# Kernel tuning notes

Hardware: AMD Instinct MI355X
Metric: run time of the kernel (lower is better)

The kernel has to match this reference:

```python
import jax, jax.numpy as jnp
import numpy as np

DIM = 128
WS = 7
NH = 8
HEAD_DIM = DIM // NH
SCALE = HEAD_DIM ** -0.5


def setup_inputs() -> dict:
    key = jax.random.key(0)
    k1, k2, k3, k4 = jax.random.split(key, 4)
    x = jax.random.normal(k1, (32, 56, 56, DIM), dtype=jnp.float32)
    qkv_w = jax.random.normal(k2, (3 * DIM, DIM), dtype=jnp.float32) * (DIM ** -0.5)
    proj_w = jax.random.normal(k3, (DIM, DIM), dtype=jnp.float32) * (DIM ** -0.5)
    proj_b = jax.random.normal(k4, (DIM,), dtype=jnp.float32) * 0.01
    return {"x": x, "qkv_w": qkv_w, "proj_w": proj_w, "proj_b": proj_b}


def reference(x, qkv_w, proj_w, proj_b):
    B, H, W, C = x.shape
    pad_b = (WS - H % WS) % WS
    pad_r = (WS - W % WS) % WS
    x = jnp.pad(x, ((0, 0), (0, pad_b), (0, pad_r), (0, 0)))
    Hp, Wp = H + pad_b, W + pad_r
    nH, nW = Hp // WS, Wp // WS
    # window partition: [B*nH*nW, WS*WS, C]
    xw = x.reshape(B, nH, WS, nW, WS, C).transpose(0, 1, 3, 2, 4, 5)
    xw = xw.reshape(B * nH * nW, WS * WS, C)
    # qkv projection (torch Linear: x @ W^T), split into heads
    qkv = (xw @ qkv_w.T).reshape(-1, WS * WS, 3, NH, HEAD_DIM)
    qkv = qkv.transpose(2, 0, 3, 1, 4)  # [3, nWin, H, T, d]
    q, k, v = qkv[0], qkv[1], qkv[2]
    attn = jax.nn.softmax(jnp.einsum('nhqd,nhkd->nhqk', q, k) * SCALE, axis=-1)
    out = jnp.einsum('nhqk,nhkd->nhqd', attn, v)
    out = out.transpose(0, 2, 1, 3).reshape(-1, WS * WS, C)
    out = out @ proj_w.T + proj_b
    # window reverse
    out = out.reshape(B, nH, nW, WS, WS, C).transpose(0, 1, 3, 2, 4, 5)
    out = out.reshape(B, Hp, Wp, C)
    return out[:, :H, :W, :]
```

## Files before the change

### kernel.cpp

```cpp
#include <hip/hip_runtime.h>

typedef unsigned short ushort_t;
typedef __attribute__((ext_vector_type(8))) short short8v;
typedef __attribute__((ext_vector_type(4))) short short4v;
typedef __attribute__((ext_vector_type(4))) float f32x4;
typedef __attribute__((ext_vector_type(2))) __bf16 bf16x2;

#define QOFF   0
#define KOFF   8704
#define AOOFF  0
#define VOFF   17408
#define SMEMSZ 26624

__device__ __forceinline__ ushort_t f2bf(float f) {
  return __builtin_bit_cast(unsigned short, (__bf16)f);
}
__device__ __forceinline__ unsigned pack2(float lo, float hi) {
  bf16x2 v; v[0] = (__bf16)lo; v[1] = (__bf16)hi;
  return __builtin_bit_cast(unsigned, v);
}

__device__ __forceinline__ f32x4 mfma16(short8v a, short8v b, f32x4 c) {
  return __builtin_amdgcn_mfma_f32_16x16x32_bf16(a, b, c, 0, 0, 0);
}

template<bool WS>
__device__ __forceinline__ short8v load_w8(const ushort_t* wsp, const float* wf, int n, int k0) {
  if constexpr (WS) {
    return *reinterpret_cast<const short8v*>(wsp + (size_t)n * 128 + k0);
  } else {
    const float* p = wf + (size_t)n * 128 + k0;
    float4 f0 = *reinterpret_cast<const float4*>(p);
    float4 f1 = *reinterpret_cast<const float4*>(p + 4);
    short8v t;
    t[0] = (short)f2bf(f0.x); t[1] = (short)f2bf(f0.y);
    t[2] = (short)f2bf(f0.z); t[3] = (short)f2bf(f0.w);
    t[4] = (short)f2bf(f1.x); t[5] = (short)f2bf(f1.y);
    t[6] = (short)f2bf(f1.z); t[7] = (short)f2bf(f1.w);
    return t;
  }
}

__global__ void cvt_w(const float* __restrict__ qw, const float* __restrict__ pw,
                      ushort_t* __restrict__ ws) {
  const int i = blockIdx.x * 256 + threadIdx.x;
  if (i < 49152) ws[i] = f2bf(qw[i]);
  if (i < 16384) ws[49152 + i] = f2bf(pw[i]);
}

template<bool WS>
__global__ __launch_bounds__(256, 2)
void winattn(const float* __restrict__ xg,
             const float* __restrict__ qw,
             const float* __restrict__ pw,
             const float* __restrict__ pb,
             const ushort_t* __restrict__ wsw,
             float* __restrict__ out) {
  __shared__ ushort_t smem[SMEMSZ];

  const int tid  = threadIdx.x;
  const int wid  = tid >> 6;
  const int lane = tid & 63;
  const int l15  = lane & 15;
  const int quad = lane >> 4;

  const int wb = blockIdx.x;
  const int b  = wb >> 6;
  const int wh = (wb >> 3) & 7;
  const int ww = wb & 7;
  const int rowbase = (b * 56 + wh * 7) * 56 + ww * 7;

  const float bias0 = pb[wid * 32 + l15];
  const float bias1 = pb[wid * 32 + 16 + l15];

  {
    const int tr = tid >> 5;
    const int c4 = tid & 31;
    #pragma unroll
    for (int it = 0; it < 8; ++it) {
      const int t = it * 8 + tr;
      uint2 pk = make_uint2(0u, 0u);
      if (t < 49) {
        const int i = t / 7, j = t - (t / 7) * 7;
        const float4 v = *reinterpret_cast<const float4*>(
            xg + (size_t)(rowbase + i * 56 + j) * 128 + c4 * 4);
        pk.x = pack2(v.x, v.y);
        pk.y = pack2(v.z, v.w);
      }
      *reinterpret_cast<uint2*>(&smem[t * 136 + c4 * 4]) = pk;
    }
  }
  __syncthreads();

  short8v a[4][4];
  #pragma unroll
  for (int qi = 0; qi < 4; ++qi)
    #pragma unroll
    for (int ks = 0; ks < 4; ++ks)
      a[qi][ks] = *reinterpret_cast<const short8v*>(
          &smem[(qi * 16 + l15) * 136 + ks * 32 + quad * 8]);
  __syncthreads();

  #pragma unroll
  for (int pass = 0; pass < 2; ++pass) {
    f32x4 acc[4][3];
    #pragma unroll
    for (int qi = 0; qi < 4; ++qi)
      #pragma unroll
      for (int ni = 0; ni < 3; ++ni)
        acc[qi][ni] = (f32x4){0.f, 0.f, 0.f, 0.f};

    #pragma unroll
    for (int nis = 0; nis < 3; ++nis) {
      const int ni = pass * 3 + nis;
      const int n  = wid * 96 + ni * 16 + l15;
      short8v bf[4];
      #pragma unroll
      for (int ks = 0; ks < 4; ++ks)
        bf[ks] = load_w8<WS>(wsw, qw, n, ks * 32 + quad * 8);
      #pragma unroll
      for (int qi = 0; qi < 4; ++qi)
        #pragma unroll
        for (int ks = 0; ks < 4; ++ks)
          acc[qi][nis] = mfma16(a[qi][ks], bf[ks], acc[qi][nis]);
    }

    #pragma unroll
    for (int nis = 0; nis < 3; ++nis) {
      const int ni    = pass * 3 + nis;
      const int obase = wid * 96 + ni * 16;
      if (obase < 256) {
        const int colo = ((obase < 128) ? QOFF : (KOFF - 128)) + obase + l15;
        #pragma unroll
        for (int qi = 0; qi < 4; ++qi)
          #pragma unroll
          for (int r = 0; r < 4; ++r)
            smem[colo + (qi * 16 + quad * 4 + r) * 136] = f2bf(acc[qi][nis][r]);
      } else {
        const int vrow = obase - 256 + l15;
        #pragma unroll
        for (int qi = 0; qi < 4; ++qi) {
          uint2 pk;
          pk.x = pack2(acc[qi][nis][0], acc[qi][nis][1]);
          pk.y = pack2(acc[qi][nis][2], acc[qi][nis][3]);
          *reinterpret_cast<uint2*>(&smem[VOFF + vrow * 72 + qi * 16 + quad * 4]) = pk;
        }
      }
    }
  }
  __syncthreads();

  f32x4 s[2][4][4];
  #pragma unroll
  for (int hh = 0; hh < 2; ++hh) {
    const int h    = wid * 2 + hh;
    const int colb = h * 16 + (quad & 1) * 8;
    const bool act = quad < 2;
    short8v aq[4], bk[4];
    #pragma unroll
    for (int qi = 0; qi < 4; ++qi) {
      short8v v = *reinterpret_cast<const short8v*>(&smem[QOFF + (qi * 16 + l15) * 136 + colb]);
      aq[qi] = act ? v : (short8v)0;
    }
    #pragma unroll
    for (int ki = 0; ki < 4; ++ki) {
      short8v v = *reinterpret_cast<const short8v*>(&smem[KOFF + (ki * 16 + l15) * 136 + colb]);
      bk[ki] = act ? v : (short8v)0;
    }
    #pragma unroll
    for (int qi = 0; qi < 4; ++qi)
      #pragma unroll
      for (int ki = 0; ki < 4; ++ki)
        s[hh][qi][ki] = mfma16(aq[qi], bk[ki], (f32x4){0.f, 0.f, 0.f, 0.f});
  }

  const float cexp = 0.3606737602222409f;
  #pragma unroll
  for (int hh = 0; hh < 2; ++hh) {
    #pragma unroll
    for (int qi = 0; qi < 4; ++qi) {
      #pragma unroll
      for (int r = 0; r < 4; ++r)
        s[hh][qi][3][r] = (l15 >= 1) ? -1e30f : s[hh][qi][3][r];
      #pragma unroll
      for (int r = 0; r < 4; ++r) {
        float sum = 0.f;
        #pragma unroll
        for (int ki = 0; ki < 4; ++ki) {
          const float e = __builtin_amdgcn_exp2f(s[hh][qi][ki][r] * cexp);
          s[hh][qi][ki][r] = e;
          sum += e;
        }
        sum += __shfl_xor(sum, 1);
        sum += __shfl_xor(sum, 2);
        sum += __shfl_xor(sum, 4);
        sum += __shfl_xor(sum, 8);
        const float rs = __builtin_amdgcn_rcpf(sum);
        #pragma unroll
        for (int ki = 0; ki < 4; ++ki) s[hh][qi][ki][r] *= rs;
      }
    }
  }
  __syncthreads();

  const int pbase = wid * 4352;
  f32x4 ov[2][4];
  #pragma unroll
  for (int hh = 0; hh < 2; ++hh) {
    #pragma unroll
    for (int qi = 0; qi < 4; ++qi)
      #pragma unroll
      for (int ki = 0; ki < 4; ++ki)
        #pragma unroll
        for (int r = 0; r < 4; ++r)
          smem[pbase + (qi * 16 + quad * 4 + r) * 68 + ki * 16 + l15] = f2bf(s[hh][qi][ki][r]);

    const int h = wid * 2 + hh;
    short8v bv[2];
    #pragma unroll
    for (int ks = 0; ks < 2; ++ks)
      bv[ks] = *reinterpret_cast<const short8v*>(
          &smem[VOFF + (h * 16 + l15) * 72 + ks * 32 + quad * 8]);
    #pragma unroll
    for (int qi = 0; qi < 4; ++qi) {
      f32x4 acc = (f32x4){0.f, 0.f, 0.f, 0.f};
      #pragma unroll
      for (int ks = 0; ks < 2; ++ks) {
        const ushort_t* pp = &smem[pbase + (qi * 16 + l15) * 68 + ks * 32 + quad * 8];
        const short4v p0 = *reinterpret_cast<const short4v*>(pp);
        const short4v p1 = *reinterpret_cast<const short4v*>(pp + 4);
        const short8v ap = {p0[0], p0[1], p0[2], p0[3], p1[0], p1[1], p1[2], p1[3]};
        acc = mfma16(ap, bv[ks], acc);
      }
      ov[hh][qi] = acc;
    }
  }
  __syncthreads();

  #pragma unroll
  for (int hh = 0; hh < 2; ++hh) {
    const int c = (wid * 2 + hh) * 16 + l15;
    #pragma unroll
    for (int qi = 0; qi < 4; ++qi)
      #pragma unroll
      for (int r = 0; r < 4; ++r)
        smem[AOOFF + (qi * 16 + quad * 4 + r) * 136 + c] = f2bf(ov[hh][qi][r]);
  }
  __syncthreads();

  short8v aa[4][4];
  #pragma unroll
  for (int qi = 0; qi < 4; ++qi)
    #pragma unroll
    for (int ks = 0; ks < 4; ++ks)
      aa[qi][ks] = *reinterpret_cast<const short8v*>(
          &smem[AOOFF + (qi * 16 + l15) * 136 + ks * 32 + quad * 8]);

  f32x4 pacc[4][2];
  #pragma unroll
  for (int qi = 0; qi < 4; ++qi)
    #pragma unroll
    for (int ni = 0; ni < 2; ++ni)
      pacc[qi][ni] = (f32x4){0.f, 0.f, 0.f, 0.f};

  #pragma unroll
  for (int ni = 0; ni < 2; ++ni) {
    const int n = wid * 32 + ni * 16 + l15;
    short8v bf[4];
    #pragma unroll
    for (int ks = 0; ks < 4; ++ks)
      bf[ks] = load_w8<WS>(wsw + 49152, pw, n, ks * 32 + quad * 8);
    #pragma unroll
    for (int qi = 0; qi < 4; ++qi)
      #pragma unroll
      for (int ks = 0; ks < 4; ++ks)
        pacc[qi][ni] = mfma16(aa[qi][ks], bf[ks], pacc[qi][ni]);
  }

  #pragma unroll
  for (int qi = 0; qi < 4; ++qi) {
    #pragma unroll
    for (int r = 0; r < 4; ++r) {
      const int q = qi * 16 + quad * 4 + r;
      if (q < 49) {
        const int i = q / 7, j = q - (q / 7) * 7;
        float* op = out + (size_t)(rowbase + i * 56 + j) * 128 + wid * 32 + l15;
        op[0]  = pacc[qi][0][r] + bias0;
        op[16] = pacc[qi][1][r] + bias1;
      }
    }
  }
}

extern "C" void kernel_launch(void* const* d_in, const int* in_sizes, int n_in,
                              void* d_out, int out_size, void* d_ws, size_t ws_size,
                              hipStream_t stream) {
  const float* x  = (const float*)d_in[0];
  const float* qw = (const float*)d_in[1];
  const float* pw = (const float*)d_in[2];
  const float* pb = (const float*)d_in[3];
  float* out      = (float*)d_out;
  ushort_t* ws    = (ushort_t*)d_ws;

  const bool use_ws = (ws_size >= (size_t)(49152 + 16384) * sizeof(ushort_t));
  if (use_ws) {
    hipLaunchKernelGGL(cvt_w, dim3(192), dim3(256), 0, stream, qw, pw, ws);
    hipLaunchKernelGGL((winattn<true>), dim3(2048), dim3(256), 0, stream,
                       x, qw, pw, pb, ws, out);
  } else {
    hipLaunchKernelGGL((winattn<false>), dim3(2048), dim3(256), 0, stream,
                       x, qw, pw, pb, (const ushort_t*)nullptr, out);
  }
}
```

Baseline: 164.7 us.

## Compute S^T via swapped MFMA operands and route softmax probabilities through lane shuffles

Swaps the QK^T MFMA operands so each lane holds a query's scores along keys, which reduces the softmax row-sum to two cross-lane shuffles. The normalized probabilities are packed to bf16 and redistributed with register shuffles into the A-operand layout for the PV MFMA, so they no longer round-trip through shared memory. This removes a block-wide barrier and the LDS write and read of P, and fuses the QK, softmax and PV stages per query tile. In exchange it adds many ds_bpermute shuffles and select instructions per tile, and the key-padding mask logic is rewritten for the transposed layout.

```diff
diff --git a/kernel.cpp b/kernel.cpp
--- a/kernel.cpp
+++ b/kernel.cpp
@@ -2,7 +2,7 @@
 
 typedef unsigned short ushort_t;
 typedef __attribute__((ext_vector_type(8))) short short8v;
-typedef __attribute__((ext_vector_type(4))) short short4v;
+typedef __attribute__((ext_vector_type(4))) int   i32x4;
 typedef __attribute__((ext_vector_type(4))) float f32x4;
 typedef __attribute__((ext_vector_type(2))) __bf16 bf16x2;
 
@@ -150,89 +150,83 @@
   }
   __syncthreads();
 
-  f32x4 s[2][4][4];
+  const float cexp = 0.3606737602222409f;
+  const int srcA = l15 + ((quad & 1) << 5);
+  const int srcB = srcA + 16;
+  const bool loq = (quad < 2);
+
+  f32x4 ov[2][4];
   #pragma unroll
   for (int hh = 0; hh < 2; ++hh) {
     const int h    = wid * 2 + hh;
     const int colb = h * 16 + (quad & 1) * 8;
     const bool act = quad < 2;
-    short8v aq[4], bk[4];
+    short8v bk[4], aq[4], bv[2];
+    #pragma unroll
+    for (int ki = 0; ki < 4; ++ki) {
+      short8v v = *reinterpret_cast<const short8v*>(&smem[KOFF + (ki * 16 + l15) * 136 + colb]);
+      bk[ki] = act ? v : (short8v)0;
+    }
     #pragma unroll
     for (int qi = 0; qi < 4; ++qi) {
       short8v v = *reinterpret_cast<const short8v*>(&smem[QOFF + (qi * 16 + l15) * 136 + colb]);
       aq[qi] = act ? v : (short8v)0;
     }
     #pragma unroll
-    for (int ki = 0; ki < 4; ++ki) {
-      short8v v = *reinterpret_cast<const short8v*>(&smem[KOFF + (ki * 16 + l15) * 136 + colb]);
-      bk[ki] = act ? v : (short8v)0;
-    }
-    #pragma unroll
-    for (int qi = 0; qi < 4; ++qi)
-      #pragma unroll
-      for (int ki = 0; ki < 4; ++ki)
-        s[hh][qi][ki] = mfma16(aq[qi], bk[ki], (f32x4){0.f, 0.f, 0.f, 0.f});
-  }
-
-  const float cexp = 0.3606737602222409f;
-  #pragma unroll
-  for (int hh = 0; hh < 2; ++hh) {
-    #pragma unroll
-    for (int qi = 0; qi < 4; ++qi) {
-      #pragma unroll
-      for (int r = 0; r < 4; ++r)
-        s[hh][qi][3][r] = (l15 >= 1) ? -1e30f : s[hh][qi][3][r];
-      #pragma unroll
-      for (int r = 0; r < 4; ++r) {
-        float sum = 0.f;
-        #pragma unroll
-        for (int ki = 0; ki < 4; ++ki) {
-          const float e = __builtin_amdgcn_exp2f(s[hh][qi][ki][r] * cexp);
-          s[hh][qi][ki][r] = e;
-          sum += e;
-        }
-        sum += __shfl_xor(sum, 1);
-        sum += __shfl_xor(sum, 2);
-        sum += __shfl_xor(sum, 4);
-        sum += __shfl_xor(sum, 8);
-        const float rs = __builtin_amdgcn_rcpf(sum);
-        #pragma unroll
-        for (int ki = 0; ki < 4; ++ki) s[hh][qi][ki][r] *= rs;
-      }
-    }
-  }
-  __syncthreads();
-
-  const int pbase = wid * 4352;
-  f32x4 ov[2][4];
-  #pragma unroll
-  for (int hh = 0; hh < 2; ++hh) {
-    #pragma unroll
-    for (int qi = 0; qi < 4; ++qi)
-      #pragma unroll
-      for (int ki = 0; ki < 4; ++ki)
-        #pragma unroll
-        for (int r = 0; r < 4; ++r)
-          smem[pbase + (qi * 16 + quad * 4 + r) * 68 + ki * 16 + l15] = f2bf(s[hh][qi][ki][r]);
-
-    const int h = wid * 2 + hh;
-    short8v bv[2];
-    #pragma unroll
     for (int ks = 0; ks < 2; ++ks)
       bv[ks] = *reinterpret_cast<const short8v*>(
           &smem[VOFF + (h * 16 + l15) * 72 + ks * 32 + quad * 8]);
+
     #pragma unroll
     for (int qi = 0; qi < 4; ++qi) {
-      f32x4 acc = (f32x4){0.f, 0.f, 0.f, 0.f};
-      #pragma unroll
-      for (int ks = 0; ks < 2; ++ks) {
-        const ushort_t* pp = &smem[pbase + (qi * 16 + l15) * 68 + ks * 32 + quad * 8];
-        const short4v p0 = *reinterpret_cast<const short4v*>(pp);
-        const short4v p1 = *reinterpret_cast<const short4v*>(pp + 4);
-        const short8v ap = {p0[0], p0[1], p0[2], p0[3], p1[0], p1[1], p1[2], p1[3]};
-        acc = mfma16(ap, bv[ks], acc);
-      }
-      ov[hh][qi] = acc;
+      f32x4 st[4];
+      #pragma unroll
+      for (int ki = 0; ki < 4; ++ki)
+        st[ki] = mfma16(bk[ki], aq[qi], (f32x4){0.f, 0.f, 0.f, 0.f});
+
+      st[3][0] = (quad == 0) ? st[3][0] : -1e30f;
+      st[3][1] = -1e30f; st[3][2] = -1e30f; st[3][3] = -1e30f;
+
+      float p[4][4];
+      float sum = 0.f;
+      #pragma unroll
+      for (int ki = 0; ki < 4; ++ki)
+        #pragma unroll
+        for (int r = 0; r < 4; ++r) {
+          const float e = __builtin_amdgcn_exp2f(st[ki][r] * cexp);
+          p[ki][r] = e;
+          sum += e;
+        }
+      sum += __shfl_xor(sum, 16);
+      sum += __shfl_xor(sum, 32);
+      const float rs = __builtin_amdgcn_rcpf(sum);
+
+      unsigned pk0x = pack2(p[0][0] * rs, p[0][1] * rs), pk0y = pack2(p[0][2] * rs, p[0][3] * rs);
+      unsigned pk1x = pack2(p[1][0] * rs, p[1][1] * rs), pk1y = pack2(p[1][2] * rs, p[1][3] * rs);
+      unsigned pk2x = pack2(p[2][0] * rs, p[2][1] * rs), pk2y = pack2(p[2][2] * rs, p[2][3] * rs);
+      unsigned pk3x = pack2(p[3][0] * rs, p[3][1] * rs), pk3y = pack2(p[3][2] * rs, p[3][3] * rs);
+
+      const unsigned s0xA = (unsigned)__shfl((int)pk0x, srcA), s0yA = (unsigned)__shfl((int)pk0y, srcA);
+      const unsigned s0xB = (unsigned)__shfl((int)pk0x, srcB), s0yB = (unsigned)__shfl((int)pk0y, srcB);
+      const unsigned s1xA = (unsigned)__shfl((int)pk1x, srcA), s1yA = (unsigned)__shfl((int)pk1y, srcA);
+      const unsigned s1xB = (unsigned)__shfl((int)pk1x, srcB), s1yB = (unsigned)__shfl((int)pk1y, srcB);
+      const unsigned s2xA = (unsigned)__shfl((int)pk2x, srcA), s2yA = (unsigned)__shfl((int)pk2y, srcA);
+      const unsigned s2xB = (unsigned)__shfl((int)pk2x, srcB), s2yB = (unsigned)__shfl((int)pk2y, srcB);
+      const unsigned s3xA = (unsigned)__shfl((int)pk3x, srcA), s3yA = (unsigned)__shfl((int)pk3y, srcA);
+      const unsigned s3xB = (unsigned)__shfl((int)pk3x, srcB), s3yB = (unsigned)__shfl((int)pk3y, srcB);
+
+      i32x4 am0, am1;
+      am0[0] = (int)(loq ? s0xA : s1xA);
+      am0[1] = (int)(loq ? s0yA : s1yA);
+      am0[2] = (int)(loq ? s0xB : s1xB);
+      am0[3] = (int)(loq ? s0yB : s1yB);
+      am1[0] = (int)(loq ? s2xA : s3xA);
+      am1[1] = (int)(loq ? s2yA : s3yA);
+      am1[2] = (int)(loq ? s2xB : s3xB);
+      am1[3] = (int)(loq ? s2yB : s3yB);
+
+      f32x4 acc = mfma16(__builtin_bit_cast(short8v, am0), bv[0], (f32x4){0.f, 0.f, 0.f, 0.f});
+      ov[hh][qi] = mfma16(__builtin_bit_cast(short8v, am1), bv[1], acc);
     }
   }
   __syncthreads();
```

Result: faster. 148.3 us (-9.9%).
